# Optimization experiments

Hardware: AMD Instinct MI355X
Metric: run time of the kernel (lower is better)

## Reference

```python
import jax, jax.numpy as jnp
import numpy as np

IMG = 224
PS = 16
G = IMG // PS          # 14
P = G * G              # 196 patches
CIN = 3
COUT = 768
B = 64


def setup_inputs() -> dict:
    key = jax.random.key(0)
    k1, k2, k3 = jax.random.split(key, 3)
    x = jax.random.normal(k1, (B, CIN, IMG, IMG), dtype=jnp.float32)
    # per-patch conv kernels, stacked: [P, COUT, CIN, PS, PS]
    W = jax.random.normal(k2, (P, COUT, CIN, PS, PS), dtype=jnp.float32) * 0.02
    b = jax.random.normal(k3, (P, COUT), dtype=jnp.float32) * 0.02
    return {"x": x, "W": W, "b": b}


def reference(x, W, b):
    # Each patch (i,j) is convolved with its own kernel at stride=PS -> a single
    # 1x1 output per patch == dot(patch_pixels, kernel). Batched as one einsum.
    Bn = x.shape[0]
    # [B, C, G, PS, G, PS] -> [B, G, G, C, PS, PS] -> [B, P, C*PS*PS]
    patches = x.reshape(Bn, CIN, G, PS, G, PS).transpose(0, 2, 4, 1, 3, 5)
    patches = patches.reshape(Bn, P, CIN * PS * PS)
    Wm = W.reshape(P, COUT, CIN * PS * PS)
    # [B, P, COUT]
    out = jnp.einsum('bpk,pok->bpo', patches, Wm) + b[None]
    # torch code cats along dim=2 (row-major patch order) then reshapes to
    # [B, COUT, G, G]; row-major patch order matches this reshape exactly.
    return out.transpose(0, 2, 1).reshape(Bn, COUT, G, G)
```

## Files before the change

kernel.cpp:

```cpp
#include <hip/hip_runtime.h>
#include <hip/hip_bf16.h>

#define IMG   224
#define PS    16
#define GDIM  14
#define NPATCH 196
#define CIN   3
#define NCOUT 768
#define NB    64
#define KDIM  768

#define BK    64
#define BN    128
#define LDA   72

using short8  = __attribute__((ext_vector_type(8))) short;
using floatx4 = __attribute__((ext_vector_type(4))) float;

static __device__ __forceinline__ short f2bf(float f) {
    __hip_bfloat16 h = __float2bfloat16(f);
    return *reinterpret_cast<short*>(&h);
}

__global__ __launch_bounds__(256)
void dynconv_gemm(const float* __restrict__ x,
                  const float* __restrict__ W,
                  const float* __restrict__ bias,
                  float* __restrict__ dst,
                  int use_ws) {
    __shared__ __align__(16) short As[NB][LDA];
    __shared__ __align__(16) short Bs[BN][LDA];

    const int tid = threadIdx.x;
    const int p   = blockIdx.x / 6;
    const int no  = blockIdx.x % 6;
    const int o0  = no * BN;

    const int gi = p / GDIM;
    const int gj = p % GDIM;

    const int lane = tid & 63;
    const int wv   = tid >> 6;
    const int row  = lane & 15;
    const int quad = lane >> 4;

    floatx4 acc[4][2] = {};

    const int c4 = (tid & 15) << 2;
    const int rb = tid >> 4;

    const float* Wp = W + ((size_t)p * NCOUT + o0) * KDIM;

    for (int kk = 0; kk < KDIM; kk += BK) {
        __syncthreads();

        {
            const int kg  = kk + c4;
            const int ch  = kg >> 8;
            const int rem = kg & 255;
            const int pi  = rem >> 4;
            const int pj  = rem & 15;
            const int rowoff = (gi * PS + pi) * IMG + gj * PS + pj;
            #pragma unroll
            for (int i = 0; i < 4; ++i) {
                const int m = rb + (i << 4);
                const float4 v = *(const float4*)(x + (size_t)(m * CIN + ch) * (IMG * IMG) + rowoff);
                short* d = &As[m][c4];
                d[0] = f2bf(v.x); d[1] = f2bf(v.y); d[2] = f2bf(v.z); d[3] = f2bf(v.w);
            }
        }

        {
            const float* wsrc = Wp + kk + c4;
            #pragma unroll
            for (int i = 0; i < 8; ++i) {
                const int n = rb + (i << 4);
                const float4 v = *(const float4*)(wsrc + (size_t)n * KDIM);
                short* d = &Bs[n][c4];
                d[0] = f2bf(v.x); d[1] = f2bf(v.y); d[2] = f2bf(v.z); d[3] = f2bf(v.w);
            }
        }

        __syncthreads();

        #pragma unroll
        for (int ks = 0; ks < 2; ++ks) {
            short8 a[4], bf[2];
            const int kofs = ks * 32 + quad * 8;
            #pragma unroll
            for (int mt = 0; mt < 4; ++mt)
                a[mt] = *(const short8*)&As[mt * 16 + row][kofs];
            #pragma unroll
            for (int nt = 0; nt < 2; ++nt)
                bf[nt] = *(const short8*)&Bs[wv * 32 + nt * 16 + row][kofs];
            #pragma unroll
            for (int mt = 0; mt < 4; ++mt)
                #pragma unroll
                for (int nt = 0; nt < 2; ++nt)
                    acc[mt][nt] = __builtin_amdgcn_mfma_f32_16x16x32_bf16(
                        a[mt], bf[nt], acc[mt][nt], 0, 0, 0);
        }
    }

    #pragma unroll
    for (int mt = 0; mt < 4; ++mt) {
        #pragma unroll
        for (int nt = 0; nt < 2; ++nt) {
            const int n = wv * 32 + nt * 16 + row;
            const int o = o0 + n;
            const float bv = bias[p * NCOUT + o];
            #pragma unroll
            for (int r = 0; r < 4; ++r) {
                const int m = mt * 16 + quad * 4 + r;
                const float val = acc[mt][nt][r] + bv;
                if (use_ws) {
                    dst[((size_t)m * NPATCH + p) * NCOUT + o] = val;
                } else {
                    dst[((size_t)m * NCOUT + o) * NPATCH + p] = val;
                }
            }
        }
    }
}

__global__ __launch_bounds__(256)
void dynconv_transpose(const float* __restrict__ ws, float* __restrict__ out) {
    __shared__ float tile[32][33];
    const int b  = blockIdx.z;
    const int p0 = blockIdx.x * 32;
    const int o0 = blockIdx.y * 32;
    const int tid = threadIdx.x;
    const int c  = tid & 31;
    const int r0 = tid >> 5;

    const float* src = ws  + (size_t)b * NPATCH * NCOUT;
    float*       dst = out + (size_t)b * NPATCH * NCOUT;

    #pragma unroll
    for (int i = 0; i < 4; ++i) {
        const int pr = p0 + r0 + i * 8;
        if (pr < NPATCH)
            tile[r0 + i * 8][c] = src[(size_t)pr * NCOUT + o0 + c];
    }
    __syncthreads();
    #pragma unroll
    for (int i = 0; i < 4; ++i) {
        const int orow = o0 + r0 + i * 8;
        const int pc = p0 + c;
        if (pc < NPATCH)
            dst[(size_t)orow * NPATCH + pc] = tile[c][r0 + i * 8];
    }
}

extern "C" void kernel_launch(void* const* d_in, const int* in_sizes, int n_in,
                              void* d_out, int out_size, void* d_ws, size_t ws_size,
                              hipStream_t stream) {
    const float* x    = (const float*)d_in[0];
    const float* W    = (const float*)d_in[1];
    const float* bias = (const float*)d_in[2];
    float* out = (float*)d_out;

    const size_t need = (size_t)NB * NPATCH * NCOUT * sizeof(float);
    const int use_ws = (d_ws != nullptr && ws_size >= need) ? 1 : 0;
    float* ws = (float*)d_ws;

    dynconv_gemm<<<dim3(NPATCH * 6), dim3(256), 0, stream>>>(
        x, W, bias, use_ws ? ws : out, use_ws);

    if (use_ws) {
        dynconv_transpose<<<dim3(7, 24, 64), dim3(256), 0, stream>>>(ws, out);
    }
}
```

Measured before the change: 671.0 us.

## Prefetch next K tile into registers, pack bf16 stores, bf16 workspace

The GEMM kernel now loads the next K slice of x and W into registers while the current slice is being multiplied, so global load latency overlaps with MFMA work. Conversion to bf16 is done in pairs and written to shared memory as 8-byte packed stores instead of scalar shorts. The intermediate workspace is stored as bf16 rather than fp32, which halves its write and read traffic, and the transpose kernel handles 64 output channels per block. The cost is extra register pressure from the prefetch buffers and an added bf16 rounding of the result before the final fp32 output.

```diff
diff --git a/kernel.cpp b/kernel.cpp
--- a/kernel.cpp
+++ b/kernel.cpp
@@ -17,16 +17,21 @@
 using short8  = __attribute__((ext_vector_type(8))) short;
 using floatx4 = __attribute__((ext_vector_type(4))) float;
 
-static __device__ __forceinline__ short f2bf(float f) {
-    __hip_bfloat16 h = __float2bfloat16(f);
-    return *reinterpret_cast<short*>(&h);
+static __device__ __forceinline__ uint2 pk4(float4 v) {
+    __hip_bfloat162 lo = __float22bfloat162_rn(make_float2(v.x, v.y));
+    __hip_bfloat162 hi = __float22bfloat162_rn(make_float2(v.z, v.w));
+    uint2 r;
+    r.x = *reinterpret_cast<unsigned int*>(&lo);
+    r.y = *reinterpret_cast<unsigned int*>(&hi);
+    return r;
 }
 
 __global__ __launch_bounds__(256)
 void dynconv_gemm(const float* __restrict__ x,
                   const float* __restrict__ W,
                   const float* __restrict__ bias,
-                  float* __restrict__ dst,
+                  __hip_bfloat16* __restrict__ ws,
+                  float* __restrict__ out,
                   int use_ws) {
     __shared__ __align__(16) short As[NB][LDA];
     __shared__ __align__(16) short Bs[BN][LDA];
@@ -51,34 +56,43 @@
 
     const float* Wp = W + ((size_t)p * NCOUT + o0) * KDIM;
 
+    float4 ra[4];
+    float4 rbv[8];
+
+    auto loadA = [&](int kk) {
+        const int kg  = kk + c4;
+        const int ch  = kg >> 8;
+        const int rem = kg & 255;
+        const int rowoff = (gi * PS + (rem >> 4)) * IMG + gj * PS + (rem & 15);
+        #pragma unroll
+        for (int i = 0; i < 4; ++i) {
+            const int m = rb + (i << 4);
+            ra[i] = *(const float4*)(x + (size_t)(m * CIN + ch) * (IMG * IMG) + rowoff);
+        }
+    };
+    auto loadB = [&](int kk) {
+        const float* wsrc = Wp + kk + c4;
+        #pragma unroll
+        for (int i = 0; i < 8; ++i)
+            rbv[i] = *(const float4*)(wsrc + (size_t)(rb + (i << 4)) * KDIM);
+    };
+
+    loadA(0);
+    loadB(0);
+
     for (int kk = 0; kk < KDIM; kk += BK) {
         __syncthreads();
 
-        {
-            const int kg  = kk + c4;
-            const int ch  = kg >> 8;
-            const int rem = kg & 255;
-            const int pi  = rem >> 4;
-            const int pj  = rem & 15;
-            const int rowoff = (gi * PS + pi) * IMG + gj * PS + pj;
-            #pragma unroll
-            for (int i = 0; i < 4; ++i) {
-                const int m = rb + (i << 4);
-                const float4 v = *(const float4*)(x + (size_t)(m * CIN + ch) * (IMG * IMG) + rowoff);
-                short* d = &As[m][c4];
-                d[0] = f2bf(v.x); d[1] = f2bf(v.y); d[2] = f2bf(v.z); d[3] = f2bf(v.w);
-            }
-        }
+        #pragma unroll
+        for (int i = 0; i < 4; ++i)
+            *(uint2*)&As[rb + (i << 4)][c4] = pk4(ra[i]);
+        #pragma unroll
+        for (int i = 0; i < 8; ++i)
+            *(uint2*)&Bs[rb + (i << 4)][c4] = pk4(rbv[i]);
 
-        {
-            const float* wsrc = Wp + kk + c4;
-            #pragma unroll
-            for (int i = 0; i < 8; ++i) {
-                const int n = rb + (i << 4);
-                const float4 v = *(const float4*)(wsrc + (size_t)n * KDIM);
-                short* d = &Bs[n][c4];
-                d[0] = f2bf(v.x); d[1] = f2bf(v.y); d[2] = f2bf(v.z); d[3] = f2bf(v.w);
-            }
+        if (kk + BK < KDIM) {
+            loadA(kk + BK);
+            loadB(kk + BK);
         }
 
         __syncthreads();
@@ -114,9 +128,9 @@
                 const int m = mt * 16 + quad * 4 + r;
                 const float val = acc[mt][nt][r] + bv;
                 if (use_ws) {
-                    dst[((size_t)m * NPATCH + p) * NCOUT + o] = val;
+                    ws[((size_t)m * NPATCH + p) * NCOUT + o] = __float2bfloat16(val);
                 } else {
-                    dst[((size_t)m * NCOUT + o) * NPATCH + p] = val;
+                    out[((size_t)m * NCOUT + o) * NPATCH + p] = val;
                 }
             }
         }
@@ -124,31 +138,40 @@
 }
 
 __global__ __launch_bounds__(256)
-void dynconv_transpose(const float* __restrict__ ws, float* __restrict__ out) {
-    __shared__ float tile[32][33];
+void dynconv_transpose(const __hip_bfloat16* __restrict__ ws,
+                       float* __restrict__ out) {
+    __shared__ float tile[32][65];
     const int b  = blockIdx.z;
     const int p0 = blockIdx.x * 32;
-    const int o0 = blockIdx.y * 32;
+    const int o0 = blockIdx.y * 64;
     const int tid = threadIdx.x;
-    const int c  = tid & 31;
-    const int r0 = tid >> 5;
 
-    const float* src = ws  + (size_t)b * NPATCH * NCOUT;
-    float*       dst = out + (size_t)b * NPATCH * NCOUT;
-
-    #pragma unroll
-    for (int i = 0; i < 4; ++i) {
-        const int pr = p0 + r0 + i * 8;
-        if (pr < NPATCH)
-            tile[r0 + i * 8][c] = src[(size_t)pr * NCOUT + o0 + c];
+    {
+        const int cc = tid & 31;
+        const int rr = tid >> 5;
+        #pragma unroll
+        for (int i = 0; i < 4; ++i) {
+            const int pr = p0 + rr + i * 8;
+            if (pr < NPATCH) {
+                const __hip_bfloat162 v = *(const __hip_bfloat162*)
+                    &ws[((size_t)b * NPATCH + pr) * NCOUT + o0 + 2 * cc];
+                tile[rr + i * 8][2 * cc]     = __bfloat162float(v.x);
+                tile[rr + i * 8][2 * cc + 1] = __bfloat162float(v.y);
+            }
+        }
     }
     __syncthreads();
-    #pragma unroll
-    for (int i = 0; i < 4; ++i) {
-        const int orow = o0 + r0 + i * 8;
+    {
+        const int c = tid & 31;
+        const int r = tid >> 5;
         const int pc = p0 + c;
-        if (pc < NPATCH)
-            dst[(size_t)orow * NPATCH + pc] = tile[c][r0 + i * 8];
+        if (pc < NPATCH) {
+            #pragma unroll
+            for (int i = 0; i < 8; ++i) {
+                const int orow = o0 + r + i * 8;
+                out[((size_t)b * NCOUT + orow) * NPATCH + pc] = tile[c][r + i * 8];
+            }
+        }
     }
 }
 
@@ -160,14 +183,14 @@
     const float* bias = (const float*)d_in[2];
     float* out = (float*)d_out;
 
-    const size_t need = (size_t)NB * NPATCH * NCOUT * sizeof(float);
+    const size_t need = (size_t)NB * NPATCH * NCOUT * sizeof(__hip_bfloat16);
     const int use_ws = (d_ws != nullptr && ws_size >= need) ? 1 : 0;
-    float* ws = (float*)d_ws;
+    __hip_bfloat16* ws = (__hip_bfloat16*)d_ws;
 
     dynconv_gemm<<<dim3(NPATCH * 6), dim3(256), 0, stream>>>(
-        x, W, bias, use_ws ? ws : out, use_ws);
+        x, W, bias, ws, out, use_ws);
 
     if (use_ws) {
-        dynconv_transpose<<<dim3(7, 24, 64), dim3(256), 0, stream>>>(ws, out);
+        dynconv_transpose<<<dim3(7, 12, 64), dim3(256), 0, stream>>>(ws, out);
     }
 }
```

Result: no change. 659.0 us (-1.8%).
